# Kernel optimization log

Hardware: AMD Instinct MI355X
Metric: run time of the kernel (lower is better)

Reference implementation:

```python
import jax, jax.numpy as jnp
import numpy as np

D = 256      # d_model
K = 8        # knn neighbors
Q = 2048     # num queries
N = 32768    # num superpoints
H = 8        # mamba heads (d_inner/head_dim)
HD = 64      # head_dim
ST = 64      # state_size
DIN = H * HD                 # 512, expand*d_model
CONV = DIN + 2 * ST          # 640
NPROJ = 2 * DIN + 2 * ST + H # 1160
HID = 1024   # ffn hidden
NL = 2       # ssm layers
KC = 4       # conv kernel


def _ln(x, eps=1e-5):
    m = x.mean(-1, keepdims=True)
    v = ((x - m) ** 2).mean(-1, keepdims=True)
    return (x - m) * jax.lax.rsqrt(v + eps)


def _silu(x):
    return x * jax.nn.sigmoid(x)


def _mamba2(x, Win, Wconv, bconv, A_log, Dh, dtb, rmsw, Wout):
    # x: [B, L, D]; faithful HF Mamba2Mixer recurrent form
    B, L, _ = x.shape
    proj = x @ Win.T  # [B,L,NPROJ]
    z, xBC, dt = jnp.split(proj, [DIN, DIN + CONV], axis=-1)
    # causal depthwise conv1d, kernel KC, left pad KC-1
    xp = jnp.pad(xBC, ((0, 0), (KC - 1, 0), (0, 0)))
    conv = sum(xp[:, j:j + L, :] * Wconv[:, j] for j in range(KC))
    xBC = _silu(conv + bconv)
    xs, Bm, Cm = jnp.split(xBC, [DIN, DIN + ST], axis=-1)
    dt = jax.nn.softplus(dt + dtb)  # [B,L,H]
    A = -jnp.exp(A_log)             # [H]
    xh = xs.reshape(B, L, H, HD)
    dA = jnp.exp(dt * A)            # [B,L,H]
    dBx = dt[..., None, None] * Bm[:, :, None, None, :] * xh[..., None]  # [B,L,H,HD,ST]

    def step(h, inp):
        dA_t, dBx_t, C_t = inp
        h = h * dA_t[..., None, None] + dBx_t
        y = jnp.einsum('bhds,bs->bhd', h, C_t)
        return h, y

    h0 = jnp.zeros((B, H, HD, ST), x.dtype)
    _, ys = jax.lax.scan(step, h0, (dA.transpose(1, 0, 2),
                                    dBx.transpose(1, 0, 2, 3, 4),
                                    Cm.transpose(1, 0, 2)))
    y = ys.transpose(1, 0, 2, 3) + Dh[None, None, :, None] * xh
    y = y.reshape(B, L, DIN) * _silu(z)  # gated RMSNorm
    y = y * jax.lax.rsqrt((y * y).mean(-1, keepdims=True) + 1e-5) * rmsw
    return y @ Wout.T


def setup_inputs() -> dict:
    key = jax.random.key(0)
    ks = jax.random.split(key, 32)
    s = 0.02
    rn = lambda i, sh: jax.random.normal(ks[i], sh, jnp.float32) * s
    inp = {
        'query': jax.random.normal(ks[0], (Q, D), jnp.float32),
        'query_pos': jax.random.uniform(ks[1], (Q, 3), jnp.float32),
        'inst_feats': jax.random.normal(ks[2], (N, D), jnp.float32),
        'sp_coords': jax.random.uniform(ks[3], (N, 3), jnp.float32),
        'w_q': rn(4, (D, D)), 'w_v': rn(5, (D, D)), 'w_o': rn(6, (D, D)),
        'w_k': rn(7, (K, D)), 'w_b': jnp.zeros((K,), jnp.float32),
        'ssm_Win': rn(8, (NL, NPROJ, D)),
        'ssm_Wconv': rn(9, (NL, CONV, KC)),
        'ssm_bconv': jnp.zeros((NL, CONV), jnp.float32),
        'ssm_Alog': jnp.log(jnp.broadcast_to(jnp.arange(1, H + 1, dtype=jnp.float32), (NL, H))),
        'ssm_D': jnp.ones((NL, H), jnp.float32),
        'ssm_dtb': jax.random.uniform(ks[10], (NL, H), jnp.float32) * 0.1,
        'ssm_rmsw': jnp.ones((NL, DIN), jnp.float32),
        'ssm_Wout': rn(11, (NL, D, DIN)),
        'ffn_w1': rn(12, (HID, D)), 'ffn_b1': jnp.zeros((HID,), jnp.float32),
        'ffn_w2': rn(13, (D, HID)), 'ffn_b2': jnp.zeros((D,), jnp.float32),
        'order': jnp.stack([jax.random.permutation(ks[14], Q),
                            jax.random.permutation(ks[15], Q)]).astype(jnp.int32),
    }
    return inp


def reference(query, query_pos, inst_feats, sp_coords,
              w_q, w_v, w_o, w_k, w_b,
              ssm_Win, ssm_Wconv, ssm_bconv, ssm_Alog, ssm_D, ssm_dtb, ssm_rmsw, ssm_Wout,
              ffn_w1, ffn_b1, ffn_w2, ffn_b2, order):
    # --- MambaAggregation: KNN group + small-K softmax mixing ---
    d2 = (query_pos ** 2).sum(-1, keepdims=True) + (sp_coords ** 2).sum(-1)[None, :] \
         - 2.0 * query_pos @ sp_coords.T  # [Q,N]
    _, idx = jax.lax.top_k(-d2, K)        # [Q,K] nearest neighbors
    feat = inst_feats[idx]                # [Q,K,D]
    q = query @ w_q.T
    v = feat @ w_v.T
    kw = jax.nn.softmax(q @ w_k.T + w_b, axis=-1)          # [Q,K]
    w = jnp.einsum('qk,qd,qkd->qd', kw, q, v)
    x = _ln(w @ w_o.T + query)

    # --- SSM: serialize along 2 orders, Mamba2 mix, unsort, average ---
    inv = jnp.argsort(order, axis=1)  # [2,Q]
    for l in range(NL):
        sc = x
        xn = _ln(x)
        xs = xn[order]  # [2,Q,D], two serialization paths as batch
        y = _mamba2(xs, ssm_Win[l], ssm_Wconv[l], ssm_bconv[l], ssm_Alog[l],
                    ssm_D[l], ssm_dtb[l], ssm_rmsw[l], ssm_Wout[l])
        back = jnp.take_along_axis(y, inv[:, :, None], axis=1)  # undo sort
        x = _ln(sc + back.mean(0))

    # --- FFN ---
    h = jax.nn.gelu(x @ ffn_w1.T + ffn_b1, approximate=False) @ ffn_w2.T + ffn_b2
    return _ln(x + h)
```

## Files before the change

kernel.cpp:

```cpp
#include <hip/hip_runtime.h>
#include <cstdint>


typedef __attribute__((ext_vector_type(8))) short bf16x8;
typedef __attribute__((ext_vector_type(4))) float f32x4;

__device__ __forceinline__ unsigned short f2bf(float f) {
  unsigned int u = __float_as_uint(f);
  u += 0x7fff + ((u >> 16) & 1);
  return (unsigned short)(u >> 16);
}
__device__ __forceinline__ float bf2f(unsigned short h) {
  return __uint_as_float(((unsigned int)h) << 16);
}

__global__ __launch_bounds__(256) void cvt_kernel(
    const float* __restrict__ src, unsigned short* __restrict__ hi,
    unsigned short* __restrict__ lo, int n4)
{
  const int i = blockIdx.x*256 + threadIdx.x;
  if (i < n4) {
    const float4 v = ((const float4*)src)[i];
    const unsigned short h0=f2bf(v.x), h1=f2bf(v.y), h2=f2bf(v.z), h3=f2bf(v.w);
    const unsigned short l0=f2bf(v.x-bf2f(h0)), l1=f2bf(v.y-bf2f(h1)),
                         l2=f2bf(v.z-bf2f(h2)), l3=f2bf(v.w-bf2f(h3));
    ((uint2*)hi)[i] = make_uint2((unsigned)h0 | ((unsigned)h1<<16),
                                 (unsigned)h2 | ((unsigned)h3<<16));
    ((uint2*)lo)[i] = make_uint2((unsigned)l0 | ((unsigned)l1<<16),
                                 (unsigned)l2 | ((unsigned)l3<<16));
  }
}

#define KNN_DECL(i)                                                            \
  unsigned int k0_##i=0xFFFFFFFFu,k1_##i=0xFFFFFFFFu,k2_##i=0xFFFFFFFFu,       \
               k3_##i=0xFFFFFFFFu,k4_##i=0xFFFFFFFFu,k5_##i=0xFFFFFFFFu,       \
               k6_##i=0xFFFFFFFFu,k7_##i=0xFFFFFFFFu;                          \
  int id0_##i=0x7fffffff,id1_##i=0x7fffffff,id2_##i=0x7fffffff,                \
      id3_##i=0x7fffffff,id4_##i=0x7fffffff,id5_##i=0x7fffffff,                \
      id6_##i=0x7fffffff,id7_##i=0x7fffffff

#define KNN_INS_Q(i, ukv, uiv)                                                 \
  do {                                                                         \
    const unsigned int _k = (ukv); const int _v = (uiv);                       \
    const bool a0 = _k < k0_##i;                                               \
    const bool a1 = _k < k1_##i;                                               \
    const bool a2 = _k < k2_##i;                                               \
    const bool a3 = _k < k3_##i;                                               \
    const bool a4 = _k < k4_##i;                                               \
    const bool a5 = _k < k5_##i;                                               \
    const bool a6 = _k < k6_##i;                                               \
    k7_##i = a6 ? k6_##i : _k;                  id7_##i = a6 ? id6_##i : _v;   \
    k6_##i = a5 ? k5_##i : (a6 ? _k : k6_##i);  id6_##i = a5 ? id5_##i : (a6 ? _v : id6_##i); \
    k5_##i = a4 ? k4_##i : (a5 ? _k : k5_##i);  id5_##i = a4 ? id4_##i : (a5 ? _v : id5_##i); \
    k4_##i = a3 ? k3_##i : (a4 ? _k : k4_##i);  id4_##i = a3 ? id3_##i : (a4 ? _v : id4_##i); \
    k3_##i = a2 ? k2_##i : (a3 ? _k : k3_##i);  id3_##i = a2 ? id2_##i : (a3 ? _v : id3_##i); \
    k2_##i = a1 ? k1_##i : (a2 ? _k : k2_##i);  id2_##i = a1 ? id1_##i : (a2 ? _v : id2_##i); \
    k1_##i = a0 ? k0_##i : (a1 ? _k : k1_##i);  id1_##i = a0 ? id0_##i : (a1 ? _v : id1_##i); \
    k0_##i = a0 ? _k : k0_##i;                  id0_##i = a0 ? _v : id0_##i;   \
  } while (0)

__device__ __forceinline__ bool ulex_less(unsigned int k, int i,
                                          unsigned int kr, int ir) {
  return k < kr || (k == kr && i < ir);
}

#define KNN_INS_LEXQ(i, ukv, uiv)                                              \
  do {                                                                         \
    const unsigned int _k = (ukv); const int _v = (uiv);                       \
    const bool a0 = ulex_less(_k, _v, k0_##i, id0_##i);                        \
    const bool a1 = ulex_less(_k, _v, k1_##i, id1_##i);                        \
    const bool a2 = ulex_less(_k, _v, k2_##i, id2_##i);                        \
    const bool a3 = ulex_less(_k, _v, k3_##i, id3_##i);                        \
    const bool a4 = ulex_less(_k, _v, k4_##i, id4_##i);                        \
    const bool a5 = ulex_less(_k, _v, k5_##i, id5_##i);                        \
    const bool a6 = ulex_less(_k, _v, k6_##i, id6_##i);                        \
    k7_##i = a6 ? k6_##i : _k;                  id7_##i = a6 ? id6_##i : _v;   \
    k6_##i = a5 ? k5_##i : (a6 ? _k : k6_##i);  id6_##i = a5 ? id5_##i : (a6 ? _v : id6_##i); \
    k5_##i = a4 ? k4_##i : (a5 ? _k : k5_##i);  id5_##i = a4 ? id4_##i : (a5 ? _v : id5_##i); \
    k4_##i = a3 ? k3_##i : (a4 ? _k : k4_##i);  id4_##i = a3 ? id3_##i : (a4 ? _v : id4_##i); \
    k3_##i = a2 ? k2_##i : (a3 ? _k : k3_##i);  id3_##i = a2 ? id2_##i : (a3 ? _v : id3_##i); \
    k2_##i = a1 ? k1_##i : (a2 ? _k : k2_##i);  id2_##i = a1 ? id1_##i : (a2 ? _v : id2_##i); \
    k1_##i = a0 ? k0_##i : (a1 ? _k : k1_##i);  id1_##i = a0 ? id0_##i : (a1 ? _v : id1_##i); \
    k0_##i = a0 ? _k : k0_##i;                  id0_##i = a0 ? _v : id0_##i;   \
  } while (0)

#define KNN_ROUND(i)                                                           \
  do {                                                                         \
    const float d2 = (qq##i + p.w)                                             \
                   - 2.0f*(qx##i*p.x + qy##i*p.y + qz##i*p.z);                 \
    unsigned int u = __float_as_uint(d2);                                      \
    u ^= (unsigned int)((int)u >> 31) | 0x80000000u;                           \
    unsigned long long m = __ballot(u < k7_##i);                               \
    while (m) {                                                                \
      const int l = __ffsll(m) - 1;                                            \
      m &= m - 1;                                                              \
      const unsigned int uk = (unsigned int)__shfl((int)u, l);                 \
      if (uk < k7_##i) KNN_INS_Q(i, uk, nb + l);                               \
    }                                                                          \
  } while (0)

#define KNN_STORE(i)                                                           \
  do {                                                                         \
    const int o = (i)*32 + wave*8;                                             \
    skey[o+0]=k0_##i; skey[o+1]=k1_##i; skey[o+2]=k2_##i; skey[o+3]=k3_##i;    \
    skey[o+4]=k4_##i; skey[o+5]=k5_##i; skey[o+6]=k6_##i; skey[o+7]=k7_##i;    \
    sidx[o+0]=id0_##i; sidx[o+1]=id1_##i; sidx[o+2]=id2_##i; sidx[o+3]=id3_##i;\
    sidx[o+4]=id4_##i; sidx[o+5]=id5_##i; sidx[o+6]=id6_##i; sidx[o+7]=id7_##i;\
  } while (0)

__global__ void prep_kernel(const float* __restrict__ spos,
                            float4* __restrict__ P4)
{
#pragma clang fp contract(off)
  const int n = blockIdx.x*256 + threadIdx.x;
  if (n < 32768) {
    const float sx = spos[n*3+0], sy = spos[n*3+1], sz = spos[n*3+2];
    P4[n] = make_float4(sx, sy, sz, sx*sx + sy*sy + sz*sz);
  }
}

__global__ __launch_bounds__(256) void knn_kernel(
    const float* __restrict__ qpos, const float4* __restrict__ P4,
    int* __restrict__ idx_out)
{
#pragma clang fp contract(off)
  __shared__ unsigned int skey[128];
  __shared__ int          sidx[128];
  const int q0 = blockIdx.x << 2, tid = threadIdx.x;
  const int wave = tid >> 6, lane = tid & 63;
  const float qx0 = qpos[(q0+0)*3+0], qy0 = qpos[(q0+0)*3+1], qz0 = qpos[(q0+0)*3+2];
  const float qx1 = qpos[(q0+1)*3+0], qy1 = qpos[(q0+1)*3+1], qz1 = qpos[(q0+1)*3+2];
  const float qx2 = qpos[(q0+2)*3+0], qy2 = qpos[(q0+2)*3+1], qz2 = qpos[(q0+2)*3+2];
  const float qx3 = qpos[(q0+3)*3+0], qy3 = qpos[(q0+3)*3+1], qz3 = qpos[(q0+3)*3+2];
  const float qq0 = qx0*qx0 + qy0*qy0 + qz0*qz0;
  const float qq1 = qx1*qx1 + qy1*qy1 + qz1*qz1;
  const float qq2 = qx2*qx2 + qy2*qy2 + qz2*qz2;
  const float qq3 = qx3*qx3 + qy3*qy3 + qz3*qz3;
  KNN_DECL(0); KNN_DECL(1); KNN_DECL(2); KNN_DECL(3);
  const int base = wave << 13;
  float4 p = P4[base + lane];
  float4 pn = p;
  for (int it = 0; it < 128; ++it) {
    if (it < 127) pn = P4[base + ((it+1) << 6) + lane];
    const int nb = base + (it << 6);
    KNN_ROUND(0); KNN_ROUND(1); KNN_ROUND(2); KNN_ROUND(3);
    p = pn;
  }
  if (lane == 0) { KNN_STORE(0); KNN_STORE(1); KNN_STORE(2); KNN_STORE(3); }
  __syncthreads();
  if (tid < 4) {
    KNN_DECL(m);
    const int o = tid*32;
    for (int s = 0; s < 32; ++s) {
      const unsigned int uk = skey[o + s];
      const int          ui = sidx[o + s];
      if (ulex_less(uk, ui, k7_m, id7_m)) KNN_INS_LEXQ(m, uk, ui);
    }
    const int ob = (q0 + tid)*8;
    idx_out[ob+0]=id0_m; idx_out[ob+1]=id1_m; idx_out[ob+2]=id2_m; idx_out[ob+3]=id3_m;
    idx_out[ob+4]=id4_m; idx_out[ob+5]=id5_m; idx_out[ob+6]=id6_m; idx_out[ob+7]=id7_m;
  }
}

__global__ void inv_kernel(const int* __restrict__ order, int* __restrict__ inv)
{
  int i = blockIdx.x*blockDim.x + threadIdx.x;
  if (i < 4096) { int b = i >> 11, t = i & 2047; inv[(b<<11) + order[i]] = t; }
}

#define GBM 128
#define GBN 64
#define GBK 32
#define GLDK 40
__global__ __launch_bounds__(256) void gemm_mfma(
    const unsigned short* __restrict__ Ahp, const unsigned short* __restrict__ Alp,
    const int* __restrict__ rowmap,
    const unsigned short* __restrict__ Bhp, const unsigned short* __restrict__ Blp,
    const float* __restrict__ bias,
    float* __restrict__ Y,
    unsigned short* __restrict__ Yh, unsigned short* __restrict__ Yl,
    int M, int Nn, int Kd, int act)
{
  __shared__ unsigned short Ah[GBM*GLDK], Al[GBM*GLDK];
  __shared__ unsigned short Bh[GBN*GLDK], Bl[GBN*GLDK];
  const int tid = threadIdx.x;
  const int bm = blockIdx.x, bn = blockIdx.y;
  const int wid = tid >> 6, lane = tid & 63;
  const int wr = wid >> 1, wc = wid & 1;
  const int l15 = lane & 15, lk = (lane >> 4) << 3;

  const int sar = tid >> 1, sak = (tid & 1) << 4;
  const int agrow = bm*GBM + sar;
  const int asrc = rowmap ? rowmap[agrow] : agrow;
  const unsigned short* ArH = Ahp + (size_t)asrc * Kd + sak;
  const unsigned short* ArL = Alp + (size_t)asrc * Kd + sak;
  const int sbr = tid >> 2, sbk = (tid & 3) << 3;
  const int wrow = bn*GBN + sbr;
  const bool bok = (wrow < Nn);
  const unsigned short* BrH = Bhp + (size_t)(bok ? wrow : 0) * Kd + sbk;
  const unsigned short* BrL = Blp + (size_t)(bok ? wrow : 0) * Kd + sbk;

  f32x4 acc[4][2];
#pragma unroll
  for (int m = 0; m < 4; ++m)
#pragma unroll
    for (int n = 0; n < 2; ++n) acc[m][n] = (f32x4){0.f,0.f,0.f,0.f};

  const uint4 z4 = make_uint4(0u,0u,0u,0u);
  for (int k0 = 0; k0 < Kd; k0 += GBK) {
    const int ao = sar*GLDK + sak;
    *(uint4*)&Ah[ao]     = *(const uint4*)(ArH + k0);
    *(uint4*)&Ah[ao + 8] = *(const uint4*)(ArH + k0 + 8);
    *(uint4*)&Al[ao]     = *(const uint4*)(ArL + k0);
    *(uint4*)&Al[ao + 8] = *(const uint4*)(ArL + k0 + 8);
    const int bo = sbr*GLDK + sbk;
    *(uint4*)&Bh[bo] = bok ? *(const uint4*)(BrH + k0) : z4;
    *(uint4*)&Bl[bo] = bok ? *(const uint4*)(BrL + k0) : z4;
    __syncthreads();
    bf16x8 afh[4], afl[4], bfh[2], bfl[2];
#pragma unroll
    for (int m = 0; m < 4; ++m) {
      const int row = wr*64 + m*16 + l15;
      afh[m] = *(const bf16x8*)&Ah[row*GLDK + lk];
      afl[m] = *(const bf16x8*)&Al[row*GLDK + lk];
    }
#pragma unroll
    for (int n = 0; n < 2; ++n) {
      const int row = wc*32 + n*16 + l15;
      bfh[n] = *(const bf16x8*)&Bh[row*GLDK + lk];
      bfl[n] = *(const bf16x8*)&Bl[row*GLDK + lk];
    }
#pragma unroll
    for (int m = 0; m < 4; ++m)
#pragma unroll
      for (int n = 0; n < 2; ++n) {
        acc[m][n] = __builtin_amdgcn_mfma_f32_16x16x32_bf16(afh[m], bfh[n], acc[m][n], 0,0,0);
        acc[m][n] = __builtin_amdgcn_mfma_f32_16x16x32_bf16(afh[m], bfl[n], acc[m][n], 0,0,0);
        acc[m][n] = __builtin_amdgcn_mfma_f32_16x16x32_bf16(afl[m], bfh[n], acc[m][n], 0,0,0);
      }
    __syncthreads();
  }
  const int crow0 = bm*GBM + wr*64 + (lane >> 4)*4;
#pragma unroll
  for (int m = 0; m < 4; ++m) {
#pragma unroll
    for (int n = 0; n < 2; ++n) {
      const int col = bn*GBN + wc*32 + n*16 + l15;
      if (col < Nn) {
#pragma unroll
        for (int r = 0; r < 4; ++r) {
          float v = acc[m][n][r];
          if (bias) v += bias[col];
          if (act == 1) v = 0.5f*v*(1.f + erff(v*0.7071067811865475f));
          const size_t idx = (size_t)(crow0 + m*16 + r)*Nn + col;
          if (Yh) {
            const unsigned short h = f2bf(v);
            Yh[idx] = h; Yl[idx] = f2bf(v - bf2f(h));
          } else {
            Y[idx] = v;
          }
        }
      }
    }
  }
}

__global__ __launch_bounds__(256) void kwmix_kernel(
    const float* __restrict__ QP, const float* __restrict__ wk,
    const float* __restrict__ wb, const float* __restrict__ V,
    unsigned short* __restrict__ Wh, unsigned short* __restrict__ Wl)
{
  const int wave = threadIdx.x >> 6, lane = threadIdx.x & 63;
  const int q = blockIdx.x*4 + wave;
  float qv[4];
#pragma unroll
  for (int j = 0; j < 4; ++j) qv[j] = QP[(size_t)q*256 + lane + 64*j];
  float logit[8];
#pragma unroll
  for (int k = 0; k < 8; ++k) {
    float p = 0.f;
#pragma unroll
    for (int j = 0; j < 4; ++j) p += qv[j]*wk[k*256 + lane + 64*j];
    for (int off = 32; off; off >>= 1) p += __shfl_xor(p, off);
    logit[k] = p + wb[k];
  }
  float mx = logit[0];
#pragma unroll
  for (int k = 1; k < 8; ++k) mx = fmaxf(mx, logit[k]);
  float e[8]; float s = 0.f;
#pragma unroll
  for (int k = 0; k < 8; ++k) { e[k] = expf(logit[k]-mx); s += e[k]; }
  float inv = 1.f/s;
  float acc[4] = {0.f,0.f,0.f,0.f};
#pragma unroll
  for (int k = 0; k < 8; ++k) {
    float kwv = e[k]*inv;
#pragma unroll
    for (int j = 0; j < 4; ++j)
      acc[j] = fmaf(kwv, V[(size_t)(q*8+k)*256 + lane + 64*j], acc[j]);
  }
#pragma unroll
  for (int j = 0; j < 4; ++j) {
    const float v = qv[j]*acc[j];
    const unsigned short h = f2bf(v);
    const size_t o = (size_t)q*256 + lane + 64*j;
    Wh[o] = h; Wl[o] = f2bf(v - bf2f(h));
  }
}

__global__ __launch_bounds__(256) void ln_kernel(
    const float* __restrict__ a, const float* __restrict__ b,
    float* __restrict__ out,
    unsigned short* __restrict__ oh, unsigned short* __restrict__ ol,
    int rows)
{
  const int wave = threadIdx.x >> 6, lane = threadIdx.x & 63;
  const int row = blockIdx.x*4 + wave;
  if (row >= rows) return;
  float v[4];
#pragma unroll
  for (int j = 0; j < 4; ++j) {
    float x = a[(size_t)row*256 + lane + 64*j];
    if (b) x += b[(size_t)row*256 + lane + 64*j];
    v[j] = x;
  }
  float s = v[0]+v[1]+v[2]+v[3];
  for (int off = 32; off; off >>= 1) s += __shfl_xor(s, off);
  float m = s * (1.0f/256.0f);
  float t = 0.f;
#pragma unroll
  for (int j = 0; j < 4; ++j) { float d = v[j]-m; t += d*d; }
  for (int off = 32; off; off >>= 1) t += __shfl_xor(t, off);
  float r = rsqrtf(t * (1.0f/256.0f) + 1e-5f);
#pragma unroll
  for (int j = 0; j < 4; ++j) {
    const float y = (v[j]-m)*r;
    const size_t o = (size_t)row*256 + lane + 64*j;
    if (out) out[o] = y;
    if (oh) { const unsigned short h = f2bf(y); oh[o] = h; ol[o] = f2bf(y - bf2f(h)); }
  }
}

__global__ __launch_bounds__(256) void ln_unsort_kernel(
    const float* __restrict__ OUTL, const int* __restrict__ INV,
    float* __restrict__ X,
    unsigned short* __restrict__ oh, unsigned short* __restrict__ ol)
{
  const int wave = threadIdx.x >> 6, lane = threadIdx.x & 63;
  const int q = blockIdx.x*4 + wave;
  const int i0 = INV[q], i1 = INV[2048 + q];
  float v[4];
#pragma unroll
  for (int j = 0; j < 4; ++j) {
    int d = lane + 64*j;
    v[j] = X[(size_t)q*256 + d]
         + 0.5f*(OUTL[(size_t)i0*256 + d] + OUTL[(size_t)(2048+i1)*256 + d]);
  }
  float s = v[0]+v[1]+v[2]+v[3];
  for (int off = 32; off; off >>= 1) s += __shfl_xor(s, off);
  float m = s * (1.0f/256.0f);
  float t = 0.f;
#pragma unroll
  for (int j = 0; j < 4; ++j) { float d = v[j]-m; t += d*d; }
  for (int off = 32; off; off >>= 1) t += __shfl_xor(t, off);
  float r = rsqrtf(t * (1.0f/256.0f) + 1e-5f);
#pragma unroll
  for (int j = 0; j < 4; ++j) {
    const float y = (v[j]-m)*r;
    const size_t o = (size_t)q*256 + lane + 64*j;
    X[o] = y;
    if (oh) { const unsigned short h = f2bf(y); oh[o] = h; ol[o] = f2bf(y - bf2f(h)); }
  }
}

__global__ void conv_kernel(const float* __restrict__ PROJ,
    const float* __restrict__ Wc, const float* __restrict__ bc,
    float* __restrict__ XBC)
{
  const int c = threadIdx.x;
  const int bt = blockIdx.x;
  const int t = bt & 2047;
  float acc = bc[c];
#pragma unroll
  for (int j = 0; j < 4; ++j) {
    int d = j - 3;
    if (t + d >= 0)
      acc = fmaf(PROJ[(size_t)(bt + d)*1160 + 512 + c], Wc[c*4+j], acc);
  }
  XBC[(size_t)bt*640 + c] = acc / (1.f + expf(-acc));
}

__global__ void dta_kernel(const float* __restrict__ PROJ,
    const float* __restrict__ dtb, const float* __restrict__ Alog,
    float* __restrict__ Ddt, float* __restrict__ Dda)
{
  const int i = blockIdx.x*256 + threadIdx.x;
  const int bt = i >> 3, hh = i & 7;
  float x = PROJ[(size_t)bt*1160 + 1152 + hh] + dtb[hh];
  float dt = (x > 20.f) ? x : log1pf(expf(x));
  float A = -expf(Alog[hh]);
  Ddt[hh*4096 + bt] = dt;
  Dda[hh*4096 + bt] = expf(dt * A);
}

__global__ __launch_bounds__(64) void scan1_kernel(
    const float* __restrict__ XBC, const float* __restrict__ Ddt,
    const float* __restrict__ Dda, float* __restrict__ SCH, float* __restrict__ PC)
{
  const int blk = blockIdx.x;
  const int c = blk & 31, hh = (blk >> 5) & 7, b = blk >> 8;
  const int lane = threadIdx.x;
  const int t0 = (b << 11) + (c << 6);
  __shared__ float Bsh[64][64];
  __shared__ float Xsh[64][64];
  __shared__ float dAs[64], dts[64];
#pragma unroll
  for (int it = 0; it < 16; ++it) {
    int idx = it*64 + lane;
    int t = idx >> 4, c4 = (idx & 15) << 2;
    *(float4*)&Bsh[t][c4] = *(const float4*)&XBC[(size_t)(t0 + t)*640 + 512 + c4];
    *(float4*)&Xsh[t][c4] = *(const float4*)&XBC[(size_t)(t0 + t)*640 + (hh<<6) + c4];
  }
  dAs[lane] = Dda[hh*4096 + t0 + lane];
  dts[lane] = Ddt[hh*4096 + t0 + lane];
  __syncthreads();
  float h[64];
#pragma unroll
  for (int s = 0; s < 64; ++s) h[s] = 0.f;
  float p = 1.f;
  for (int t = 0; t < 64; ++t) {
    const float dA = dAs[t];
    const float u = dts[t]*Xsh[t][lane];
    p *= dA;
    const float4* B4 = (const float4*)&Bsh[t][0];
#pragma unroll
    for (int s4 = 0; s4 < 16; ++s4) {
      float4 bv = B4[s4];
      h[4*s4+0] = fmaf(h[4*s4+0], dA, bv.x*u);
      h[4*s4+1] = fmaf(h[4*s4+1], dA, bv.y*u);
      h[4*s4+2] = fmaf(h[4*s4+2], dA, bv.z*u);
      h[4*s4+3] = fmaf(h[4*s4+3], dA, bv.w*u);
    }
  }
  float* op = SCH + (size_t)blk*4096 + lane*64;
#pragma unroll
  for (int s4 = 0; s4 < 16; ++s4)
    ((float4*)op)[s4] = make_float4(h[4*s4], h[4*s4+1], h[4*s4+2], h[4*s4+3]);
  if (lane == 0) PC[blk] = p;
}

__global__ void combine_kernel(float* __restrict__ SCH, const float* __restrict__ PC)
{
  const int tid = blockIdx.x*256 + threadIdx.x;
  const int bh = tid >> 12, ds = tid & 4095;
  float h = 0.f;
  for (int cc = 0; cc < 32; ++cc) {
    size_t o = ((size_t)(bh*32 + cc) << 12) + ds;
    float s = SCH[o];
    SCH[o] = h;
    h = fmaf(h, PC[bh*32+cc], s);
  }
}

__global__ __launch_bounds__(64) void scan2_kernel(
    const float* __restrict__ XBC, const float* __restrict__ Ddt,
    const float* __restrict__ Dda, const float* __restrict__ HST,
    const float* __restrict__ Dm, float* __restrict__ Yout)
{
  const int blk = blockIdx.x;
  const int c = blk & 31, hh = (blk >> 5) & 7, b = blk >> 8;
  const int lane = threadIdx.x;
  const int t0 = (b << 11) + (c << 6);
  __shared__ float Bsh[64][64];
  __shared__ float Csh[64][64];
  __shared__ float Xsh[64][64];
  __shared__ float dAs[64], dts[64];
#pragma unroll
  for (int it = 0; it < 16; ++it) {
    int idx = it*64 + lane;
    int t = idx >> 4, c4 = (idx & 15) << 2;
    *(float4*)&Bsh[t][c4] = *(const float4*)&XBC[(size_t)(t0 + t)*640 + 512 + c4];
    *(float4*)&Csh[t][c4] = *(const float4*)&XBC[(size_t)(t0 + t)*640 + 576 + c4];
    *(float4*)&Xsh[t][c4] = *(const float4*)&XBC[(size_t)(t0 + t)*640 + (hh<<6) + c4];
  }
  dAs[lane] = Dda[hh*4096 + t0 + lane];
  dts[lane] = Ddt[hh*4096 + t0 + lane];
  const float Dh = Dm[hh];
  float h[64];
  const float4* hp = (const float4*)(HST + (size_t)blk*4096 + lane*64);
#pragma unroll
  for (int s4 = 0; s4 < 16; ++s4) {
    float4 t4 = hp[s4];
    h[4*s4+0]=t4.x; h[4*s4+1]=t4.y; h[4*s4+2]=t4.z; h[4*s4+3]=t4.w;
  }
  __syncthreads();
  for (int t = 0; t < 64; ++t) {
    const float dA = dAs[t];
    const float u = dts[t]*Xsh[t][lane];
    float y = 0.f;
    const float4* B4 = (const float4*)&Bsh[t][0];
    const float4* C4 = (const float4*)&Csh[t][0];
#pragma unroll
    for (int s4 = 0; s4 < 16; ++s4) {
      float4 bv = B4[s4];
      float4 cv = C4[s4];
      h[4*s4+0] = fmaf(h[4*s4+0], dA, bv.x*u); y = fmaf(cv.x, h[4*s4+0], y);
      h[4*s4+1] = fmaf(h[4*s4+1], dA, bv.y*u); y = fmaf(cv.y, h[4*s4+1], y);
      h[4*s4+2] = fmaf(h[4*s4+2], dA, bv.z*u); y = fmaf(cv.z, h[4*s4+2], y);
      h[4*s4+3] = fmaf(h[4*s4+3], dA, bv.w*u); y = fmaf(cv.w, h[4*s4+3], y);
    }
    Yout[(size_t)(t0 + t)*512 + (hh<<6) + lane] = y + Dh*Xsh[t][lane];
  }
}

__global__ __launch_bounds__(256) void gaterms_kernel(
    const float* __restrict__ Y, const float* __restrict__ PROJ,
    const float* __restrict__ rmsw,
    unsigned short* __restrict__ Oh, unsigned short* __restrict__ Ol)
{
  const int wave = threadIdx.x >> 6, lane = threadIdx.x & 63;
  const int row = blockIdx.x*4 + wave;
  float v[8]; float ss = 0.f;
#pragma unroll
  for (int j = 0; j < 8; ++j) {
    float y = Y[(size_t)row*512 + lane + 64*j];
    float z = PROJ[(size_t)row*1160 + lane + 64*j];
    float g = y * (z / (1.f + expf(-z)));
    v[j] = g; ss += g*g;
  }
  for (int off = 32; off; off >>= 1) ss += __shfl_xor(ss, off);
  float r = rsqrtf(ss * (1.0f/512.0f) + 1e-5f);
#pragma unroll
  for (int j = 0; j < 8; ++j) {
    const float o = v[j] * r * rmsw[lane + 64*j];
    const unsigned short h = f2bf(o);
    const size_t ix = (size_t)row*512 + lane + 64*j;
    Oh[ix] = h; Ol[ix] = f2bf(o - bf2f(h));
  }
}

extern "C" void kernel_launch(void* const* d_in, const int* in_sizes, int n_in,
                              void* d_out, int out_size, void* d_ws, size_t ws_size,
                              hipStream_t stream)
{
  (void)in_sizes; (void)n_in; (void)out_size; (void)ws_size;
  const float* query = (const float*)d_in[0];
  const float* qpos  = (const float*)d_in[1];
  const float* feats = (const float*)d_in[2];
  const float* spos  = (const float*)d_in[3];
  const float* w_q   = (const float*)d_in[4];
  const float* w_v   = (const float*)d_in[5];
  const float* w_o   = (const float*)d_in[6];
  const float* w_k   = (const float*)d_in[7];
  const float* w_b   = (const float*)d_in[8];
  const float* Win   = (const float*)d_in[9];
  const float* Wconv = (const float*)d_in[10];
  const float* bconv = (const float*)d_in[11];
  const float* Alog  = (const float*)d_in[12];
  const float* Dm    = (const float*)d_in[13];
  const float* dtb   = (const float*)d_in[14];
  const float* rmsw  = (const float*)d_in[15];
  const float* Wout  = (const float*)d_in[16];
  const float* fw1   = (const float*)d_in[17];
  const float* fb1   = (const float*)d_in[18];
  const float* fw2   = (const float*)d_in[19];
  const float* fb2   = (const float*)d_in[20];
  const int*   order = (const int*)d_in[21];
  float* out = (float*)d_out;

  char* ws = (char*)d_ws;
  size_t off = 0;
  auto alloc = [&](size_t bytes) -> void* {
    void* p = ws + off;
    off = (off + bytes + 255) & ~(size_t)255;
    return p;
  };
  int*   IDX = (int*)alloc((size_t)2048*8*4);
  int*   INV = (int*)alloc((size_t)4096*4);
  float* PC  = (float*)alloc((size_t)512*4);
  float4* P4 = (float4*)alloc((size_t)32768*16);
  float* Ddt = (float*)alloc((size_t)4096*8*4);
  float* Dda = (float*)alloc((size_t)4096*8*4);
  float* QP  = (float*)alloc((size_t)2048*256*4);
  float* WO  = (float*)alloc((size_t)2048*256*4);
  float* X   = (float*)alloc((size_t)2048*256*4);
  float* U1  = (float*)alloc((size_t)4096*1160*4);
  float* U2  = (float*)alloc((size_t)4096*640*4);
  float* SCH = (float*)alloc((size_t)512*4096*4);
  float* Yb  = (float*)alloc((size_t)4096*512*4);
  float* U6  = (float*)alloc((size_t)4096*256*4);
  unsigned short* Qh  = (unsigned short*)alloc((size_t)2048*256*2);
  unsigned short* Ql  = (unsigned short*)alloc((size_t)2048*256*2);
  unsigned short* U7h = (unsigned short*)alloc((size_t)32768*256*2);
  unsigned short* U7l = (unsigned short*)alloc((size_t)32768*256*2);
  unsigned short* WBh = (unsigned short*)alloc((size_t)2048*256*2);
  unsigned short* WBl = (unsigned short*)alloc((size_t)2048*256*2);
  unsigned short* XNh = (unsigned short*)alloc((size_t)2048*256*2);
  unsigned short* XNl = (unsigned short*)alloc((size_t)2048*256*2);
  unsigned short* Ybh = (unsigned short*)alloc((size_t)4096*512*2);
  unsigned short* Ybl = (unsigned short*)alloc((size_t)4096*512*2);
  unsigned short* Xh  = (unsigned short*)alloc((size_t)2048*256*2);
  unsigned short* Xl  = (unsigned short*)alloc((size_t)2048*256*2);
  unsigned short* Wqh = (unsigned short*)alloc((size_t)256*256*2);
  unsigned short* Wql = (unsigned short*)alloc((size_t)256*256*2);
  unsigned short* Wvh = (unsigned short*)alloc((size_t)256*256*2);
  unsigned short* Wvl = (unsigned short*)alloc((size_t)256*256*2);
  unsigned short* Woh = (unsigned short*)alloc((size_t)256*256*2);
  unsigned short* Wol = (unsigned short*)alloc((size_t)256*256*2);
  unsigned short* Wih = (unsigned short*)alloc((size_t)2*1160*256*2);
  unsigned short* Wil = (unsigned short*)alloc((size_t)2*1160*256*2);
  unsigned short* Wuh = (unsigned short*)alloc((size_t)2*256*512*2);
  unsigned short* Wul = (unsigned short*)alloc((size_t)2*256*512*2);
  unsigned short* F1h = (unsigned short*)alloc((size_t)1024*256*2);
  unsigned short* F1l = (unsigned short*)alloc((size_t)1024*256*2);
  unsigned short* F2h = (unsigned short*)alloc((size_t)256*1024*2);
  unsigned short* F2l = (unsigned short*)alloc((size_t)256*1024*2);
  float* Vb   = U1;  float* PROJ = U1;
  float* XBC  = U2;
  float* OUTL = U6;  float* FFO  = U6;
  unsigned short* FFHh = U7h;
  unsigned short* FFHl = U7l;

  auto cvt = [&](const float* s, unsigned short* h, unsigned short* l, int n) {
    cvt_kernel<<<(n/4 + 255)/256, 256, 0, stream>>>(s, h, l, n/4);
  };

  inv_kernel<<<16, 256, 0, stream>>>(order, INV);
  prep_kernel<<<128, 256, 0, stream>>>(spos, P4);
  knn_kernel<<<512, 256, 0, stream>>>(qpos, P4, IDX);
  cvt(query, Qh, Ql, 2048*256);
  cvt(feats, U7h, U7l, 32768*256);
  cvt(w_q, Wqh, Wql, 256*256);
  cvt(w_v, Wvh, Wvl, 256*256);
  cvt(w_o, Woh, Wol, 256*256);
  cvt(Win, Wih, Wil, 2*1160*256);
  cvt(Wout, Wuh, Wul, 2*256*512);
  cvt(fw1, F1h, F1l, 1024*256);
  cvt(fw2, F2h, F2l, 256*1024);
  gemm_mfma<<<dim3(16,4), 256, 0, stream>>>(Qh, Ql, nullptr, Wqh, Wql, nullptr,
                                            QP, nullptr, nullptr, 2048,256,256,0);
  gemm_mfma<<<dim3(128,4), 256, 0, stream>>>(U7h, U7l, IDX, Wvh, Wvl, nullptr,
                                             Vb, nullptr, nullptr, 16384,256,256,0);
  kwmix_kernel<<<512, 256, 0, stream>>>(QP, w_k, w_b, Vb, WBh, WBl);
  gemm_mfma<<<dim3(16,4), 256, 0, stream>>>(WBh, WBl, nullptr, Woh, Wol, nullptr,
                                            WO, nullptr, nullptr, 2048,256,256,0);
  ln_kernel<<<512, 256, 0, stream>>>(WO, query, X, nullptr, nullptr, 2048);

  for (int l = 0; l < 2; ++l) {
    ln_kernel<<<512, 256, 0, stream>>>(X, nullptr, nullptr, XNh, XNl, 2048);
    gemm_mfma<<<dim3(32,19), 256, 0, stream>>>(XNh, XNl, order,
                                               Wih + (size_t)l*1160*256,
                                               Wil + (size_t)l*1160*256,
                                               nullptr, PROJ, nullptr, nullptr,
                                               4096,1160,256,0);
    conv_kernel<<<4096, 640, 0, stream>>>(PROJ, Wconv + l*640*4, bconv + l*640, XBC);
    dta_kernel<<<128, 256, 0, stream>>>(PROJ, dtb + l*8, Alog + l*8, Ddt, Dda);
    scan1_kernel<<<512, 64, 0, stream>>>(XBC, Ddt, Dda, SCH, PC);
    combine_kernel<<<256, 256, 0, stream>>>(SCH, PC);
    scan2_kernel<<<512, 64, 0, stream>>>(XBC, Ddt, Dda, SCH, Dm + l*8, Yb);
    gaterms_kernel<<<1024, 256, 0, stream>>>(Yb, PROJ, rmsw + l*512, Ybh, Ybl);
    gemm_mfma<<<dim3(32,4), 256, 0, stream>>>(Ybh, Ybl, nullptr,
                                              Wuh + (size_t)l*256*512,
                                              Wul + (size_t)l*256*512,
                                              nullptr, OUTL, nullptr, nullptr,
                                              4096,256,512,0);
    ln_unsort_kernel<<<512, 256, 0, stream>>>(OUTL, INV, X,
                                              (l==1) ? Xh : nullptr,
                                              (l==1) ? Xl : nullptr);
  }

  gemm_mfma<<<dim3(16,16), 256, 0, stream>>>(Xh, Xl, nullptr, F1h, F1l, fb1,
                                             nullptr, FFHh, FFHl, 2048,1024,256,1);
  gemm_mfma<<<dim3(16,4), 256, 0, stream>>>(FFHh, FFHl, nullptr, F2h, F2l, fb2,
                                            FFO, nullptr, nullptr, 2048,256,1024,0);
  ln_kernel<<<512, 256, 0, stream>>>(FFO, X, out, nullptr, nullptr, 2048);
}
```

Baseline: 607.4 us.

## Use one query per KNN block and widen GEMM N-tile to 128

The KNN kernel now handles one query per block (2048 blocks) instead of four, and compares float distances directly rather than order-preserving unsigned keys. It also drops the software prefetch of the next point batch. Separately, the MFMA GEMM tile grows from 128x64 to 128x128, each wave computes 4x4 fragments, and every GEMM grid's N dimension is halved to match. The aim is more parallelism and latency hiding in KNN and more reuse of A tiles per block in the GEMMs, at the cost of more registers and fewer blocks for the small GEMMs.

```diff
diff --git a/kernel.cpp b/kernel.cpp
--- a/kernel.cpp
+++ b/kernel.cpp
@@ -31,81 +31,54 @@
   }
 }
 
-#define KNN_DECL(i)                                                            \
-  unsigned int k0_##i=0xFFFFFFFFu,k1_##i=0xFFFFFFFFu,k2_##i=0xFFFFFFFFu,       \
-               k3_##i=0xFFFFFFFFu,k4_##i=0xFFFFFFFFu,k5_##i=0xFFFFFFFFu,       \
-               k6_##i=0xFFFFFFFFu,k7_##i=0xFFFFFFFFu;                          \
-  int id0_##i=0x7fffffff,id1_##i=0x7fffffff,id2_##i=0x7fffffff,                \
-      id3_##i=0x7fffffff,id4_##i=0x7fffffff,id5_##i=0x7fffffff,                \
-      id6_##i=0x7fffffff,id7_##i=0x7fffffff
-
-#define KNN_INS_Q(i, ukv, uiv)                                                 \
+__device__ __forceinline__ bool flex_less(float d, int i, float dr, int ir) {
+  return d < dr || (d == dr && i < ir);
+}
+
+#define KNN_INS_F(dv, iv)                                                      \
   do {                                                                         \
-    const unsigned int _k = (ukv); const int _v = (uiv);                       \
-    const bool a0 = _k < k0_##i;                                               \
-    const bool a1 = _k < k1_##i;                                               \
-    const bool a2 = _k < k2_##i;                                               \
-    const bool a3 = _k < k3_##i;                                               \
-    const bool a4 = _k < k4_##i;                                               \
-    const bool a5 = _k < k5_##i;                                               \
-    const bool a6 = _k < k6_##i;                                               \
-    k7_##i = a6 ? k6_##i : _k;                  id7_##i = a6 ? id6_##i : _v;   \
-    k6_##i = a5 ? k5_##i : (a6 ? _k : k6_##i);  id6_##i = a5 ? id5_##i : (a6 ? _v : id6_##i); \
-    k5_##i = a4 ? k4_##i : (a5 ? _k : k5_##i);  id5_##i = a4 ? id4_##i : (a5 ? _v : id5_##i); \
-    k4_##i = a3 ? k3_##i : (a4 ? _k : k4_##i);  id4_##i = a3 ? id3_##i : (a4 ? _v : id4_##i); \
-    k3_##i = a2 ? k2_##i : (a3 ? _k : k3_##i);  id3_##i = a2 ? id2_##i : (a3 ? _v : id3_##i); \
-    k2_##i = a1 ? k1_##i : (a2 ? _k : k2_##i);  id2_##i = a1 ? id1_##i : (a2 ? _v : id2_##i); \
-    k1_##i = a0 ? k0_##i : (a1 ? _k : k1_##i);  id1_##i = a0 ? id0_##i : (a1 ? _v : id1_##i); \
-    k0_##i = a0 ? _k : k0_##i;                  id0_##i = a0 ? _v : id0_##i;   \
+    const float _d = (dv); const int _v = (iv);                                \
+    const bool a0 = _d < bd0;                                                  \
+    const bool a1 = _d < bd1;                                                  \
+    const bool a2 = _d < bd2;                                                  \
+    const bool a3 = _d < bd3;                                                  \
+    const bool a4 = _d < bd4;                                                  \
+    const bool a5 = _d < bd5;                                                  \
+    const bool a6 = _d < bd6;                                                  \
+    bd7 = a6 ? bd6 : _d;              id7 = a6 ? id6 : _v;                     \
+    bd6 = a5 ? bd5 : (a6 ? _d : bd6); id6 = a5 ? id5 : (a6 ? _v : id6);        \
+    bd5 = a4 ? bd4 : (a5 ? _d : bd5); id5 = a4 ? id4 : (a5 ? _v : id5);        \
+    bd4 = a3 ? bd3 : (a4 ? _d : bd4); id4 = a3 ? id3 : (a4 ? _v : id4);        \
+    bd3 = a2 ? bd2 : (a3 ? _d : bd3); id3 = a2 ? id2 : (a3 ? _v : id3);        \
+    bd2 = a1 ? bd1 : (a2 ? _d : bd2); id2 = a1 ? id1 : (a2 ? _v : id2);        \
+    bd1 = a0 ? bd0 : (a1 ? _d : bd1); id1 = a0 ? id0 : (a1 ? _v : id1);        \
+    bd0 = a0 ? _d : bd0;              id0 = a0 ? _v : id0;                     \
   } while (0)
 
-__device__ __forceinline__ bool ulex_less(unsigned int k, int i,
-                                          unsigned int kr, int ir) {
-  return k < kr || (k == kr && i < ir);
-}
-
-#define KNN_INS_LEXQ(i, ukv, uiv)                                              \
+#define KNN_INS_FLEX(dv, iv)                                                   \
   do {                                                                         \
-    const unsigned int _k = (ukv); const int _v = (uiv);                       \
-    const bool a0 = ulex_less(_k, _v, k0_##i, id0_##i);                        \
-    const bool a1 = ulex_less(_k, _v, k1_##i, id1_##i);                        \
-    const bool a2 = ulex_less(_k, _v, k2_##i, id2_##i);                        \
-    const bool a3 = ulex_less(_k, _v, k3_##i, id3_##i);                        \
-    const bool a4 = ulex_less(_k, _v, k4_##i, id4_##i);                        \
-    const bool a5 = ulex_less(_k, _v, k5_##i, id5_##i);                        \
-    const bool a6 = ulex_less(_k, _v, k6_##i, id6_##i);                        \
-    k7_##i = a6 ? k6_##i : _k;                  id7_##i = a6 ? id6_##i : _v;   \
-    k6_##i = a5 ? k5_##i : (a6 ? _k : k6_##i);  id6_##i = a5 ? id5_##i : (a6 ? _v : id6_##i); \
-    k5_##i = a4 ? k4_##i : (a5 ? _k : k5_##i);  id5_##i = a4 ? id4_##i : (a5 ? _v : id5_##i); \
-    k4_##i = a3 ? k3_##i : (a4 ? _k : k4_##i);  id4_##i = a3 ? id3_##i : (a4 ? _v : id4_##i); \
-    k3_##i = a2 ? k2_##i : (a3 ? _k : k3_##i);  id3_##i = a2 ? id2_##i : (a3 ? _v : id3_##i); \
-    k2_##i = a1 ? k1_##i : (a2 ? _k : k2_##i);  id2_##i = a1 ? id1_##i : (a2 ? _v : id2_##i); \
-    k1_##i = a0 ? k0_##i : (a1 ? _k : k1_##i);  id1_##i = a0 ? id0_##i : (a1 ? _v : id1_##i); \
-    k0_##i = a0 ? _k : k0_##i;                  id0_##i = a0 ? _v : id0_##i;   \
+    const float _d = (dv); const int _v = (iv);                                \
+    const bool a0 = flex_less(_d, _v, bd0, id0);                               \
+    const bool a1 = flex_less(_d, _v, bd1, id1);                               \
+    const bool a2 = flex_less(_d, _v, bd2, id2);                               \
+    const bool a3 = flex_less(_d, _v, bd3, id3);                               \
+    const bool a4 = flex_less(_d, _v, bd4, id4);                               \
+    const bool a5 = flex_less(_d, _v, bd5, id5);                               \
+    const bool a6 = flex_less(_d, _v, bd6, id6);                               \
+    bd7 = a6 ? bd6 : _d;              id7 = a6 ? id6 : _v;                     \
+    bd6 = a5 ? bd5 : (a6 ? _d : bd6); id6 = a5 ? id5 : (a6 ? _v : id6);        \
+    bd5 = a4 ? bd4 : (a5 ? _d : bd5); id5 = a4 ? id4 : (a5 ? _v : id5);        \
+    bd4 = a3 ? bd3 : (a4 ? _d : bd4); id4 = a3 ? id3 : (a4 ? _v : id4);        \
+    bd3 = a2 ? bd2 : (a3 ? _d : bd3); id3 = a2 ? id2 : (a3 ? _v : id3);        \
+    bd2 = a1 ? bd1 : (a2 ? _d : bd2); id2 = a1 ? id1 : (a2 ? _v : id2);        \
+    bd1 = a0 ? bd0 : (a1 ? _d : bd1); id1 = a0 ? id0 : (a1 ? _v : id1);        \
+    bd0 = a0 ? _d : bd0;              id0 = a0 ? _v : id0;                     \
   } while (0)
 
-#define KNN_ROUND(i)                                                           \
+#define KNN_RESET_F()                                                          \
   do {                                                                         \
-    const float d2 = (qq##i + p.w)                                             \
-                   - 2.0f*(qx##i*p.x + qy##i*p.y + qz##i*p.z);                 \
-    unsigned int u = __float_as_uint(d2);                                      \
-    u ^= (unsigned int)((int)u >> 31) | 0x80000000u;                           \
-    unsigned long long m = __ballot(u < k7_##i);                               \
-    while (m) {                                                                \
-      const int l = __ffsll(m) - 1;                                            \
-      m &= m - 1;                                                              \
-      const unsigned int uk = (unsigned int)__shfl((int)u, l);                 \
-      if (uk < k7_##i) KNN_INS_Q(i, uk, nb + l);                               \
-    }                                                                          \
-  } while (0)
-
-#define KNN_STORE(i)                                                           \
-  do {                                                                         \
-    const int o = (i)*32 + wave*8;                                             \
-    skey[o+0]=k0_##i; skey[o+1]=k1_##i; skey[o+2]=k2_##i; skey[o+3]=k3_##i;    \
-    skey[o+4]=k4_##i; skey[o+5]=k5_##i; skey[o+6]=k6_##i; skey[o+7]=k7_##i;    \
-    sidx[o+0]=id0_##i; sidx[o+1]=id1_##i; sidx[o+2]=id2_##i; sidx[o+3]=id3_##i;\
-    sidx[o+4]=id4_##i; sidx[o+5]=id5_##i; sidx[o+6]=id6_##i; sidx[o+7]=id7_##i;\
+    bd0=bd1=bd2=bd3=bd4=bd5=bd6=bd7 = 3.4e38f;                                 \
+    id0=id1=id2=id3=id4=id5=id6=id7 = 0x7fffffff;                              \
   } while (0)
 
 __global__ void prep_kernel(const float* __restrict__ spos,
@@ -124,41 +97,46 @@
     int* __restrict__ idx_out)
 {
 #pragma clang fp contract(off)
-  __shared__ unsigned int skey[128];
-  __shared__ int          sidx[128];
-  const int q0 = blockIdx.x << 2, tid = threadIdx.x;
+  __shared__ float skey[32];
+  __shared__ int   sidx[32];
+  const int q = blockIdx.x, tid = threadIdx.x;
   const int wave = tid >> 6, lane = tid & 63;
-  const float qx0 = qpos[(q0+0)*3+0], qy0 = qpos[(q0+0)*3+1], qz0 = qpos[(q0+0)*3+2];
-  const float qx1 = qpos[(q0+1)*3+0], qy1 = qpos[(q0+1)*3+1], qz1 = qpos[(q0+1)*3+2];
-  const float qx2 = qpos[(q0+2)*3+0], qy2 = qpos[(q0+2)*3+1], qz2 = qpos[(q0+2)*3+2];
-  const float qx3 = qpos[(q0+3)*3+0], qy3 = qpos[(q0+3)*3+1], qz3 = qpos[(q0+3)*3+2];
-  const float qq0 = qx0*qx0 + qy0*qy0 + qz0*qz0;
-  const float qq1 = qx1*qx1 + qy1*qy1 + qz1*qz1;
-  const float qq2 = qx2*qx2 + qy2*qy2 + qz2*qz2;
-  const float qq3 = qx3*qx3 + qy3*qy3 + qz3*qz3;
-  KNN_DECL(0); KNN_DECL(1); KNN_DECL(2); KNN_DECL(3);
-  const int base = wave << 13;
-  float4 p = P4[base + lane];
-  float4 pn = p;
+  const float qx = qpos[q*3+0], qy = qpos[q*3+1], qz = qpos[q*3+2];
+  const float qq = qx*qx + qy*qy + qz*qz;
+  float bd0,bd1,bd2,bd3,bd4,bd5,bd6,bd7;
+  int   id0,id1,id2,id3,id4,id5,id6,id7;
+  KNN_RESET_F();
+  const float4* pp = P4 + (wave << 13) + lane;
+  int nb = (wave << 13);
   for (int it = 0; it < 128; ++it) {
-    if (it < 127) pn = P4[base + ((it+1) << 6) + lane];
-    const int nb = base + (it << 6);
-    KNN_ROUND(0); KNN_ROUND(1); KNN_ROUND(2); KNN_ROUND(3);
-    p = pn;
-  }
-  if (lane == 0) { KNN_STORE(0); KNN_STORE(1); KNN_STORE(2); KNN_STORE(3); }
+    const float4 p = *pp;  pp += 64;
+    const float d2 = (qq + p.w) - 2.0f*(qx*p.x + qy*p.y + qz*p.z);
+    unsigned long long m = __ballot(d2 < bd7);
+    while (m) {
+      const int l = __ffsll(m) - 1;
+      m &= m - 1;
+      const float dk = __shfl(d2, l);
+      if (dk < bd7) KNN_INS_F(dk, nb + l);
+    }
+    nb += 64;
+  }
+  if (lane == 0) {
+    const int o = wave*8;
+    skey[o+0]=bd0; skey[o+1]=bd1; skey[o+2]=bd2; skey[o+3]=bd3;
+    skey[o+4]=bd4; skey[o+5]=bd5; skey[o+6]=bd6; skey[o+7]=bd7;
+    sidx[o+0]=id0; sidx[o+1]=id1; sidx[o+2]=id2; sidx[o+3]=id3;
+    sidx[o+4]=id4; sidx[o+5]=id5; sidx[o+6]=id6; sidx[o+7]=id7;
+  }
   __syncthreads();
-  if (tid < 4) {
-    KNN_DECL(m);
-    const int o = tid*32;
+  if (tid == 0) {
+    KNN_RESET_F();
     for (int s = 0; s < 32; ++s) {
-      const unsigned int uk = skey[o + s];
-      const int          ui = sidx[o + s];
-      if (ulex_less(uk, ui, k7_m, id7_m)) KNN_INS_LEXQ(m, uk, ui);
+      const float dk = skey[s];
+      const int   ui = sidx[s];
+      if (flex_less(dk, ui, bd7, id7)) KNN_INS_FLEX(dk, ui);
     }
-    const int ob = (q0 + tid)*8;
-    idx_out[ob+0]=id0_m; idx_out[ob+1]=id1_m; idx_out[ob+2]=id2_m; idx_out[ob+3]=id3_m;
-    idx_out[ob+4]=id4_m; idx_out[ob+5]=id5_m; idx_out[ob+6]=id6_m; idx_out[ob+7]=id7_m;
+    idx_out[q*8+0]=id0; idx_out[q*8+1]=id1; idx_out[q*8+2]=id2; idx_out[q*8+3]=id3;
+    idx_out[q*8+4]=id4; idx_out[q*8+5]=id5; idx_out[q*8+6]=id6; idx_out[q*8+7]=id7;
   }
 }
 
@@ -169,7 +147,7 @@
 }
 
 #define GBM 128
-#define GBN 64
+#define GBN 128
 #define GBK 32
 #define GLDK 40
 __global__ __launch_bounds__(256) void gemm_mfma(
@@ -189,35 +167,35 @@
   const int wr = wid >> 1, wc = wid & 1;
   const int l15 = lane & 15, lk = (lane >> 4) << 3;
 
-  const int sar = tid >> 1, sak = (tid & 1) << 4;
-  const int agrow = bm*GBM + sar;
+  const int srow = tid >> 1, sk = (tid & 1) << 4;
+  const int agrow = bm*GBM + srow;
   const int asrc = rowmap ? rowmap[agrow] : agrow;
-  const unsigned short* ArH = Ahp + (size_t)asrc * Kd + sak;
-  const unsigned short* ArL = Alp + (size_t)asrc * Kd + sak;
-  const int sbr = tid >> 2, sbk = (tid & 3) << 3;
-  const int wrow = bn*GBN + sbr;
+  const unsigned short* ArH = Ahp + (size_t)asrc * Kd + sk;
+  const unsigned short* ArL = Alp + (size_t)asrc * Kd + sk;
+  const int wrow = bn*GBN + srow;
   const bool bok = (wrow < Nn);
-  const unsigned short* BrH = Bhp + (size_t)(bok ? wrow : 0) * Kd + sbk;
-  const unsigned short* BrL = Blp + (size_t)(bok ? wrow : 0) * Kd + sbk;
-
-  f32x4 acc[4][2];
+  const unsigned short* BrH = Bhp + (size_t)(bok ? wrow : 0) * Kd + sk;
+  const unsigned short* BrL = Blp + (size_t)(bok ? wrow : 0) * Kd + sk;
+
+  f32x4 acc[4][4];
 #pragma unroll
   for (int m = 0; m < 4; ++m)
 #pragma unroll
-    for (int n = 0; n < 2; ++n) acc[m][n] = (f32x4){0.f,0.f,0.f,0.f};
+    for (int n = 0; n < 4; ++n) acc[m][n] = (f32x4){0.f,0.f,0.f,0.f};
 
   const uint4 z4 = make_uint4(0u,0u,0u,0u);
   for (int k0 = 0; k0 < Kd; k0 += GBK) {
-    const int ao = sar*GLDK + sak;
-    *(uint4*)&Ah[ao]     = *(const uint4*)(ArH + k0);
-    *(uint4*)&Ah[ao + 8] = *(const uint4*)(ArH + k0 + 8);
-    *(uint4*)&Al[ao]     = *(const uint4*)(ArL + k0);
-    *(uint4*)&Al[ao + 8] = *(const uint4*)(ArL + k0 + 8);
-    const int bo = sbr*GLDK + sbk;
-    *(uint4*)&Bh[bo] = bok ? *(const uint4*)(BrH + k0) : z4;
-    *(uint4*)&Bl[bo] = bok ? *(const uint4*)(BrL + k0) : z4;
+    const int so = srow*GLDK + sk;
+    *(uint4*)&Ah[so]     = *(const uint4*)(ArH + k0);
+    *(uint4*)&Ah[so + 8] = *(const uint4*)(ArH + k0 + 8);
+    *(uint4*)&Al[so]     = *(const uint4*)(ArL + k0);
+    *(uint4*)&Al[so + 8] = *(const uint4*)(ArL + k0 + 8);
+    *(uint4*)&Bh[so]     = bok ? *(const uint4*)(BrH + k0)     : z4;
+    *(uint4*)&Bh[so + 8] = bok ? *(const uint4*)(BrH + k0 + 8) : z4;
+    *(uint4*)&Bl[so]     = bok ? *(const uint4*)(BrL + k0)     : z4;
+    *(uint4*)&Bl[so + 8] = bok ? *(const uint4*)(BrL + k0 + 8) : z4;
     __syncthreads();
-    bf16x8 afh[4], afl[4], bfh[2], bfl[2];
+    bf16x8 afh[4], afl[4], bfh[4], bfl[4];
 #pragma unroll
     for (int m = 0; m < 4; ++m) {
       const int row = wr*64 + m*16 + l15;
@@ -225,15 +203,15 @@
       afl[m] = *(const bf16x8*)&Al[row*GLDK + lk];
     }
 #pragma unroll
-    for (int n = 0; n < 2; ++n) {
-      const int row = wc*32 + n*16 + l15;
+    for (int n = 0; n < 4; ++n) {
+      const int row = wc*64 + n*16 + l15;
       bfh[n] = *(const bf16x8*)&Bh[row*GLDK + lk];
       bfl[n] = *(const bf16x8*)&Bl[row*GLDK + lk];
     }
 #pragma unroll
     for (int m = 0; m < 4; ++m)
 #pragma unroll
-      for (int n = 0; n < 2; ++n) {
+      for (int n = 0; n < 4; ++n) {
         acc[m][n] = __builtin_amdgcn_mfma_f32_16x16x32_bf16(afh[m], bfh[n], acc[m][n], 0,0,0);
         acc[m][n] = __builtin_amdgcn_mfma_f32_16x16x32_bf16(afh[m], bfl[n], acc[m][n], 0,0,0);
         acc[m][n] = __builtin_amdgcn_mfma_f32_16x16x32_bf16(afl[m], bfh[n], acc[m][n], 0,0,0);
@@ -244,8 +222,8 @@
 #pragma unroll
   for (int m = 0; m < 4; ++m) {
 #pragma unroll
-    for (int n = 0; n < 2; ++n) {
-      const int col = bn*GBN + wc*32 + n*16 + l15;
+    for (int n = 0; n < 4; ++n) {
+      const int col = bn*GBN + wc*64 + n*16 + l15;
       if (col < Nn) {
 #pragma unroll
         for (int r = 0; r < 4; ++r) {
@@ -627,7 +605,7 @@
 
   inv_kernel<<<16, 256, 0, stream>>>(order, INV);
   prep_kernel<<<128, 256, 0, stream>>>(spos, P4);
-  knn_kernel<<<512, 256, 0, stream>>>(qpos, P4, IDX);
+  knn_kernel<<<2048, 256, 0, stream>>>(qpos, P4, IDX);
   cvt(query, Qh, Ql, 2048*256);
   cvt(feats, U7h, U7l, 32768*256);
   cvt(w_q, Wqh, Wql, 256*256);
@@ -637,18 +615,18 @@
   cvt(Wout, Wuh, Wul, 2*256*512);
   cvt(fw1, F1h, F1l, 1024*256);
   cvt(fw2, F2h, F2l, 256*1024);
-  gemm_mfma<<<dim3(16,4), 256, 0, stream>>>(Qh, Ql, nullptr, Wqh, Wql, nullptr,
+  gemm_mfma<<<dim3(16,2), 256, 0, stream>>>(Qh, Ql, nullptr, Wqh, Wql, nullptr,
                                             QP, nullptr, nullptr, 2048,256,256,0);
-  gemm_mfma<<<dim3(128,4), 256, 0, stream>>>(U7h, U7l, IDX, Wvh, Wvl, nullptr,
+  gemm_mfma<<<dim3(128,2), 256, 0, stream>>>(U7h, U7l, IDX, Wvh, Wvl, nullptr,
                                              Vb, nullptr, nullptr, 16384,256,256,0);
   kwmix_kernel<<<512, 256, 0, stream>>>(QP, w_k, w_b, Vb, WBh, WBl);
-  gemm_mfma<<<dim3(16,4), 256, 0, stream>>>(WBh, WBl, nullptr, Woh, Wol, nullptr,
+  gemm_mfma<<<dim3(16,2), 256, 0, stream>>>(WBh, WBl, nullptr, Woh, Wol, nullptr,
                                             WO, nullptr, nullptr, 2048,256,256,0);
   ln_kernel<<<512, 256, 0, stream>>>(WO, query, X, nullptr, nullptr, 2048);
 
   for (int l = 0; l < 2; ++l) {
     ln_kernel<<<512, 256, 0, stream>>>(X, nullptr, nullptr, XNh, XNl, 2048);
-    gemm_mfma<<<dim3(32,19), 256, 0, stream>>>(XNh, XNl, order,
+    gemm_mfma<<<dim3(32,10), 256, 0, stream>>>(XNh, XNl, order,
                                                Wih + (size_t)l*1160*256,
                                                Wil + (size_t)l*1160*256,
                                                nullptr, PROJ, nullptr, nullptr,
@@ -659,7 +637,7 @@
     combine_kernel<<<256, 256, 0, stream>>>(SCH, PC);
     scan2_kernel<<<512, 64, 0, stream>>>(XBC, Ddt, Dda, SCH, Dm + l*8, Yb);
     gaterms_kernel<<<1024, 256, 0, stream>>>(Yb, PROJ, rmsw + l*512, Ybh, Ybl);
-    gemm_mfma<<<dim3(32,4), 256, 0, stream>>>(Ybh, Ybl, nullptr,
+    gemm_mfma<<<dim3(32,2), 256, 0, stream>>>(Ybh, Ybl, nullptr,
                                               Wuh + (size_t)l*256*512,
                                               Wul + (size_t)l*256*512,
                                               nullptr, OUTL, nullptr, nullptr,
@@ -669,9 +647,9 @@
                                               (l==1) ? Xl : nullptr);
   }
 
-  gemm_mfma<<<dim3(16,16), 256, 0, stream>>>(Xh, Xl, nullptr, F1h, F1l, fb1,
-                                             nullptr, FFHh, FFHl, 2048,1024,256,1);
-  gemm_mfma<<<dim3(16,4), 256, 0, stream>>>(FFHh, FFHl, nullptr, F2h, F2l, fb2,
+  gemm_mfma<<<dim3(16,8), 256, 0, stream>>>(Xh, Xl, nullptr, F1h, F1l, fb1,
+                                            nullptr, FFHh, FFHl, 2048,1024,256,1);
+  gemm_mfma<<<dim3(16,2), 256, 0, stream>>>(FFHh, FFHl, nullptr, F2h, F2l, fb2,
                                             FFO, nullptr, nullptr, 2048,256,1024,0);
   ln_kernel<<<512, 256, 0, stream>>>(FFO, X, out, nullptr, nullptr, 2048);
 }
```

Result: slower. 658.9 us (+8.5%).
